# Performance work log

Measured on AMD Instinct MI355X. Metric: run time of the kernel, lower is better.

Reference implementation:

```python
import jax, jax.numpy as jnp
import numpy as np

B, NW = 1024, 300
N = NW // 3          # 100 tokens (keypoints)
E = 5                # token dim after cat of PE(2): 3 + 2
H, D, L = 4, 64, 3   # heads, d_attention, layers


def setup_inputs() -> dict:
    key = jax.random.key(0)
    ks = jax.random.split(key, 8)
    s = jnp.float32(0.1)
    x = jax.random.normal(ks[0], (B, NW), dtype=jnp.float32)
    Wq = jax.random.normal(ks[1], (L, H, D, E), dtype=jnp.float32) * s  # per-head W_Q (no bias)
    Wk = jax.random.normal(ks[2], (L, H, D, E), dtype=jnp.float32) * s
    Wv = jax.random.normal(ks[3], (L, H, D, E), dtype=jnp.float32) * s
    Wo = jax.random.normal(ks[4], (L, E, H * D), dtype=jnp.float32) * s  # MHA output proj (no bias)
    Wf = jax.random.normal(ks[5], (L, E, E), dtype=jnp.float32) * s      # FFN linear
    bf = jax.random.normal(ks[6], (L, E), dtype=jnp.float32) * s
    g1 = jnp.ones((L, E), dtype=jnp.float32)
    b1 = jnp.zeros((L, E), dtype=jnp.float32)
    g2 = jnp.ones((L, E), dtype=jnp.float32)
    b2 = jnp.zeros((L, E), dtype=jnp.float32)
    return dict(x=x, Wq=Wq, Wk=Wk, Wv=Wv, Wo=Wo, Wf=Wf, bf=bf,
                g1=g1, b1=b1, g2=g2, b2=b2)


def _layer_norm(x, g, b, eps=1e-5):
    mu = jnp.mean(x, axis=-1, keepdims=True)
    var = jnp.mean((x - mu) ** 2, axis=-1, keepdims=True)  # biased, like torch LN
    return (x - mu) / jnp.sqrt(var + eps) * g + b


def reference(x, Wq, Wk, Wv, Wo, Wf, bf, g1, b1, g2, b2):
    kp = x.reshape(B, N, 3)                      # 'b (n d) -> b n d', d=3
    mask = kp[:, :, -1] > 0                      # [B,N] keypoint confidence mask
    # PositionalEncoding(d_model=2, kind='cat'): div_term=[1] -> pe=[sin(pos),cos(pos)]
    pos = jnp.arange(N, dtype=jnp.float32)
    pe = jnp.stack([jnp.sin(pos), jnp.cos(pos)], axis=-1)         # [N,2]
    out = jnp.concatenate([kp, jnp.broadcast_to(pe, (B, N, 2))], axis=-1)  # [B,N,5]
    out = jnp.where(mask[:, :, None], out, jnp.float32(0.0))      # out[~mask]=0

    pair = mask[:, None, None, :] & mask[:, None, :, None]        # [B,1,N,N]
    neg = -jnp.finfo(jnp.float32).max
    scale = jnp.float32(1.0 / np.sqrt(D))
    for l in range(L):
        # per-head projections (heads vectorized over h)
        q = jnp.einsum('bne,hde->bhnd', out, Wq[l])
        k = jnp.einsum('bne,hde->bhnd', out, Wk[l])
        v = jnp.einsum('bne,hde->bhnd', out, Wv[l])
        dots = jnp.einsum('bhid,bhjd->bhij', q, k) * scale        # [B,H,N,N]
        dots = jnp.where(pair, dots, neg)
        attn = jax.nn.softmax(dots, axis=-1)
        o = jnp.einsum('bhij,bhjd->bhid', attn, v)                # [B,H,N,D]
        o = o.transpose(0, 2, 1, 3).reshape(B, N, H * D)          # concat heads
        attn_out = o @ Wo[l].T                                    # [B,N,E]
        ln1 = _layer_norm(attn_out + out, g1[l], b1[l])
        ffn = jax.nn.relu(ln1 @ Wf[l].T + bf[l])
        out = _layer_norm(ffn + ln1, g2[l], b2[l])
    return out
```

## Files before the change

kernel.cpp:

```cpp
#include <hip/hip_runtime.h>
#include <math.h>

#define NTOK 100
#define EDIM 5
#define NH   4
#define NL   3
#define DD   64
#define BLK  256

__device__ __forceinline__ float fexp2(float x){ float r; asm("v_exp_f32 %0, %1" : "=v"(r) : "v"(x)); return r; }
__device__ __forceinline__ float frcp (float x){ float r; asm("v_rcp_f32 %0, %1" : "=v"(r) : "v"(x)); return r; }
__device__ __forceinline__ float frsq (float x){ float r; asm("v_rsq_f32 %0, %1" : "=v"(r) : "v"(x)); return r; }
#define RL(v, l) __int_as_float(__builtin_amdgcn_readlane(__float_as_int(v), (l)))

__global__ void precompute_mp(const float* __restrict__ Wq,
                              const float* __restrict__ Wk,
                              const float* __restrict__ Wv,
                              const float* __restrict__ Wo,
                              float* __restrict__ mp) {
  const int blk = blockIdx.x;
  const int which = blk / 12;
  const int rem = blk % 12;
  const int l = rem / 4, h = rem % 4;
  const int t = threadIdx.x;

  __shared__ float A[320];
  __shared__ float Bsh[320];

  const float* wa = (which ? Wv : Wq) + (l*NH + h)*DD*EDIM;
  for (int r = t; r < 320; r += 64) A[r] = wa[r];
  if (which == 0) {
    const float* wk = Wk + (l*NH + h)*DD*EDIM;
    for (int r = t; r < 320; r += 64) Bsh[r] = wk[r];
  } else {
    for (int r = t; r < 320; r += 64) {
      int f = r >> 6, d = r & 63;
      Bsh[r] = Wo[(l*EDIM + f)*(NH*DD) + h*DD + d];
    }
  }
  __syncthreads();
  if (t < 25) {
    int e = t / 5, f = t % 5;
    float acc = 0.f;
    if (which == 0) {
      #pragma unroll 8
      for (int d = 0; d < DD; ++d) acc += A[d*5+e] * Bsh[d*5+f];
      acc *= 0.125f * 1.44269504088896340736f;
    } else {
      #pragma unroll 8
      for (int d = 0; d < DD; ++d) acc += A[d*5+e] * Bsh[f*64+d];
    }
    mp[which*960 + ((l*NH + h)*EDIM + e)*8 + f] = acc;
  }
}

__global__ __launch_bounds__(BLK, 4) void encoder_kernel(
    const float* __restrict__ x,
    const float* __restrict__ mp,
    const float* __restrict__ Wf,
    const float* __restrict__ bfv,
    const float* __restrict__ g1,
    const float* __restrict__ b1,
    const float* __restrict__ g2,
    const float* __restrict__ b2,
    float* __restrict__ out)
{
  const int b = blockIdx.x, t = threadIdx.x;
  const int wv = t >> 6, ln = t & 63;

  __shared__ float4 s_MP4[480];
  __shared__ float4 s_wp4[2][NH][104];
  __shared__ float  s_wp1[2][NH][104];
  __shared__ float4 s_i4[104];
  __shared__ float  s_i1[104];
  __shared__ int    s_cidx[NTOK];
  __shared__ unsigned long long s_bal[2];

  const float* mpf = (const float*)s_MP4;
  for (int r = t; r < 480; r += BLK) s_MP4[r] = ((const float4*)mp)[r];
  for (int r = t; r < 104; r += BLK) { s_i4[r] = make_float4(0.f,0.f,0.f,0.f); s_i1[r] = 0.f; }

  float k0=0.f, k1=0.f, k2=0.f, msk=0.f;
  if (t < NTOK) {
    k0 = x[b*300 + 3*t];
    k1 = x[b*300 + 3*t + 1];
    k2 = x[b*300 + 3*t + 2];
    msk = (k2 > 0.f) ? 1.f : 0.f;
  }
  unsigned long long bal = __ballot(t < NTOK && msk != 0.f);
  if (t == 0)  s_bal[0] = bal;
  if (t == 64) s_bal[1] = bal;
  __syncthreads();
  const unsigned long long bw0 = s_bal[0], bw1 = s_bal[1];
  const int nm = __builtin_amdgcn_readfirstlane(__popcll(bw0) + __popcll(bw1));
  if (t < NTOK) {
    int lane = t & 63;
    unsigned long long lm = (lane == 0) ? 0ull : ((1ull << lane) - 1ull);
    int pre = (t < 64) ? __popcll(bw0 & lm) : (__popcll(bw0) + __popcll(bw1 & lm));
    if (msk != 0.f) {
      s_i4[pre] = make_float4(k0, k1, k2, __sinf((float)t));
      s_i1[pre] = __cosf((float)t);
      s_cidx[t] = pre;
    } else {
      s_cidx[t] = nm;
    }
  }
  __syncthreads();

  const int rows = nm + 1;
  const bool twoRows = (rows > 64);
  const int jhiA = (nm < 64) ? nm : 64;
  const float wext = (float)(NTOK - nm);

  float oA0,oA1,oA2,oA3,oA4, oB0,oB1,oB2,oB3,oB4;
  { float4 v = s_i4[ln]; oA0=v.x; oA1=v.y; oA2=v.z; oA3=v.w; oA4=s_i1[ln]; }
  if (twoRows && ln < 40) {
    float4 v = s_i4[ln+64]; oB0=v.x; oB1=v.y; oB2=v.z; oB3=v.w; oB4=s_i1[ln+64];
  } else { oB0=0.f; oB1=0.f; oB2=0.f; oB3=0.f; oB4=0.f; }

  int bufp = 0;

  for (int l = 0; l < NL; ++l) {
    const float* Mh = mpf + ((l*NH + wv)*EDIM)*8;
    const float* Ph = mpf + 960 + ((l*NH + wv)*EDIM)*8;

    auto attn_row = [&](float o0,float o1,float o2,float o3,float o4,int row) {
      float oc[5] = {o0,o1,o2,o3,o4};
      float a0=0.f,a1=0.f,a2=0.f,a3=0.f,a4=0.f;
      #pragma unroll
      for (int e = 0; e < 5; ++e) {
        float4 mr = *(const float4*)(Mh + e*8); float m4 = Mh[e*8+4];
        a0 += oc[e]*mr.x; a1 += oc[e]*mr.y; a2 += oc[e]*mr.z;
        a3 += oc[e]*mr.w; a4 += oc[e]*m4;
      }
      const bool rep = (row == nm);
      if (rep) { a0=0.f; a1=0.f; a2=0.f; a3=0.f; a4=0.f; }
      float ls=0.f, w0=0.f, w1=0.f, w2=0.f, w3=0.f, w4=0.f;
      #pragma unroll 4
      for (int j = 0; j < jhiA; ++j) {
        float ox = RL(oA0,j), oy = RL(oA1,j), oz = RL(oA2,j),
              ow = RL(oA3,j), oe = RL(oA4,j);
        float s = (a0*ox + a1*oy) + ((a2*oz + a3*ow) + a4*oe);
        float p = fexp2(s);
        ls += p;
        w0 += p*ox; w1 += p*oy; w2 += p*oz; w3 += p*ow; w4 += p*oe;
      }
      if (twoRows) {
        #pragma unroll 4
        for (int j = 64; j < nm; ++j) {
          int jl = j - 64;
          float ox = RL(oB0,jl), oy = RL(oB1,jl), oz = RL(oB2,jl),
                ow = RL(oB3,jl), oe = RL(oB4,jl);
          float s = (a0*ox + a1*oy) + ((a2*oz + a3*ow) + a4*oe);
          float p = fexp2(s);
          ls += p;
          w0 += p*ox; w1 += p*oy; w2 += p*oz; w3 += p*ow; w4 += p*oe;
        }
      }
      if (rep) {
        w0 += wext*o0; w1 += wext*o1; w2 += wext*o2; w3 += wext*o3; w4 += wext*o4;
      }
      float inv = rep ? 0.01f : frcp(ls);
      float wc[5] = {w0*inv, w1*inv, w2*inv, w3*inv, w4*inv};
      float c0=0.f,c1=0.f,c2=0.f,c3=0.f,c4=0.f;
      #pragma unroll
      for (int e = 0; e < 5; ++e) {
        float4 pr = *(const float4*)(Ph + e*8); float p4 = Ph[e*8+4];
        c0 += wc[e]*pr.x; c1 += wc[e]*pr.y; c2 += wc[e]*pr.z;
        c3 += wc[e]*pr.w; c4 += wc[e]*p4;
      }
      if (row < rows) {
        s_wp4[bufp][wv][row] = make_float4(c0,c1,c2,c3);
        s_wp1[bufp][wv][row] = c4;
      }
    };

    attn_row(oA0,oA1,oA2,oA3,oA4, ln);
    if (twoRows) attn_row(oB0,oB1,oB2,oB3,oB4, ln+64);
    __syncthreads();

    auto upd = [&](float& p0,float& p1,float& p2,float& p3,float& p4,int row) {
      if (row >= rows) return;
      float y0=p0, y1=p1, y2=p2, y3=p3, y4=p4;
      #pragma unroll
      for (int hh = 0; hh < NH; ++hh) {
        float4 wA = s_wp4[bufp][hh][row];
        y0 += wA.x; y1 += wA.y; y2 += wA.z; y3 += wA.w;
        y4 += s_wp1[bufp][hh][row];
      }
      float yv[5] = {y0,y1,y2,y3,y4};
      float mu = 0.2f*(y0+y1+y2+y3+y4);
      float var = 0.f;
      #pragma unroll
      for (int e = 0; e < 5; ++e) { float d = yv[e]-mu; var += d*d; }
      float iv = frsq(var*0.2f + 1e-5f);
      float l1[5];
      #pragma unroll
      for (int e = 0; e < 5; ++e) l1[e] = (yv[e]-mu)*iv*g1[l*5+e] + b1[l*5+e];
      float r2[5];
      #pragma unroll
      for (int e = 0; e < 5; ++e) {
        float acc = bfv[l*5+e];
        #pragma unroll
        for (int f = 0; f < 5; ++f) acc += l1[f]*Wf[(l*5+e)*5+f];
        acc = acc > 0.f ? acc : 0.f;
        r2[e] = acc + l1[e];
      }
      float mu2 = 0.2f*(r2[0]+r2[1]+r2[2]+r2[3]+r2[4]);
      float var2 = 0.f;
      #pragma unroll
      for (int e = 0; e < 5; ++e) { float d = r2[e]-mu2; var2 += d*d; }
      float iv2 = frsq(var2*0.2f + 1e-5f);
      p0 = (r2[0]-mu2)*iv2*g2[l*5+0] + b2[l*5+0];
      p1 = (r2[1]-mu2)*iv2*g2[l*5+1] + b2[l*5+1];
      p2 = (r2[2]-mu2)*iv2*g2[l*5+2] + b2[l*5+2];
      p3 = (r2[3]-mu2)*iv2*g2[l*5+3] + b2[l*5+3];
      p4 = (r2[4]-mu2)*iv2*g2[l*5+4] + b2[l*5+4];
    };
    upd(oA0,oA1,oA2,oA3,oA4, ln);
    if (twoRows) upd(oB0,oB1,oB2,oB3,oB4, ln+64);
    bufp ^= 1;
  }

  if (wv == 0) {
    if (ln < rows) { s_i4[ln] = make_float4(oA0,oA1,oA2,oA3); s_i1[ln] = oA4; }
    if (twoRows && (ln + 64 < rows)) {
      s_i4[ln+64] = make_float4(oB0,oB1,oB2,oB3); s_i1[ln+64] = oB4;
    }
  }
  __syncthreads();
  for (int r = t; r < NTOK*EDIM; r += BLK) {
    int i = r / EDIM;
    int e = r - i*EDIM;
    int c = s_cidx[i];
    float v = (e < 4) ? ((const float*)&s_i4[c])[e] : s_i1[c];
    out[b*(NTOK*EDIM) + r] = v;
  }
}

extern "C" void kernel_launch(void* const* d_in, const int* in_sizes, int n_in,
                              void* d_out, int out_size, void* d_ws, size_t ws_size,
                              hipStream_t stream) {
  const float* x  = (const float*)d_in[0];
  const float* Wq = (const float*)d_in[1];
  const float* Wk = (const float*)d_in[2];
  const float* Wv = (const float*)d_in[3];
  const float* Wo = (const float*)d_in[4];
  const float* Wf = (const float*)d_in[5];
  const float* bf = (const float*)d_in[6];
  const float* g1 = (const float*)d_in[7];
  const float* b1 = (const float*)d_in[8];
  const float* g2 = (const float*)d_in[9];
  const float* b2 = (const float*)d_in[10];
  float* outp = (float*)d_out;
  float* mp   = (float*)d_ws;

  precompute_mp<<<24, 64, 0, stream>>>(Wq, Wk, Wv, Wo, mp);
  encoder_kernel<<<1024, BLK, 0, stream>>>(x, mp, Wf, bf, g1, b1, g2, b2, outp);
}
```

Measured before the change: 128.8 us.

## Process two heads per wave with 128-thread blocks and cache LN/FFN params in LDS

Halves the block to two waves, each computing two attention heads per row and sharing the readlane broadcasts and key loads across both heads. The cross-wave reduction now reads only the partner wave's partial sum from LDS and keeps its own in registers. Small FFN and LayerNorm parameters are staged into shared memory instead of being read from global memory per row. The doubled per-lane work raises register pressure and gives fewer waves per block to hide latency, and the second-row work is limited to lanes below 40.

```diff
diff --git a/kernel.cpp b/kernel.cpp
--- a/kernel.cpp
+++ b/kernel.cpp
@@ -6,7 +6,7 @@
 #define NH   4
 #define NL   3
 #define DD   64
-#define BLK  256
+#define BLK  128
 
 __device__ __forceinline__ float fexp2(float x){ float r; asm("v_exp_f32 %0, %1" : "=v"(r) : "v"(x)); return r; }
 __device__ __forceinline__ float frcp (float x){ float r; asm("v_rcp_f32 %0, %1" : "=v"(r) : "v"(x)); return r; }
@@ -54,7 +54,7 @@
   }
 }
 
-__global__ __launch_bounds__(BLK, 4) void encoder_kernel(
+__global__ __launch_bounds__(BLK, 2) void encoder_kernel(
     const float* __restrict__ x,
     const float* __restrict__ mp,
     const float* __restrict__ Wf,
@@ -69,16 +69,27 @@
   const int wv = t >> 6, ln = t & 63;
 
   __shared__ float4 s_MP4[480];
-  __shared__ float4 s_wp4[2][NH][104];
-  __shared__ float  s_wp1[2][NH][104];
+  __shared__ float4 s_wp4[2][2][104];
+  __shared__ float  s_wp1[2][2][104];
   __shared__ float4 s_i4[104];
   __shared__ float  s_i1[104];
+  __shared__ float  s_cf[152];
   __shared__ int    s_cidx[NTOK];
   __shared__ unsigned long long s_bal[2];
 
   const float* mpf = (const float*)s_MP4;
   for (int r = t; r < 480; r += BLK) s_MP4[r] = ((const float4*)mp)[r];
   for (int r = t; r < 104; r += BLK) { s_i4[r] = make_float4(0.f,0.f,0.f,0.f); s_i1[r] = 0.f; }
+  for (int r = t; r < 150; r += BLK) {
+    float v;
+    if      (r <  75) v = Wf[r];
+    else if (r <  90) v = bfv[r-75];
+    else if (r < 105) v = g1[r-90];
+    else if (r < 120) v = b1[r-105];
+    else if (r < 135) v = g2[r-120];
+    else              v = b2[r-135];
+    s_cf[r] = v;
+  }
 
   float k0=0.f, k1=0.f, k2=0.f, msk=0.f;
   if (t < NTOK) {
@@ -119,31 +130,45 @@
   } else { oB0=0.f; oB1=0.f; oB2=0.f; oB3=0.f; oB4=0.f; }
 
   int bufp = 0;
+  float cSA[5], cSB[5];
 
   for (int l = 0; l < NL; ++l) {
-    const float* Mh = mpf + ((l*NH + wv)*EDIM)*8;
-    const float* Ph = mpf + 960 + ((l*NH + wv)*EDIM)*8;
-
-    auto attn_row = [&](float o0,float o1,float o2,float o3,float o4,int row) {
+    const float* M0 = mpf + ((l*NH + 2*wv    )*EDIM)*8;
+    const float* M1 = mpf + ((l*NH + 2*wv + 1)*EDIM)*8;
+    const float* P0 = mpf + 960 + ((l*NH + 2*wv    )*EDIM)*8;
+    const float* P1 = mpf + 960 + ((l*NH + 2*wv + 1)*EDIM)*8;
+
+    auto attn_row = [&](float o0,float o1,float o2,float o3,float o4,
+                        int row, float (&cS)[5]) {
       float oc[5] = {o0,o1,o2,o3,o4};
-      float a0=0.f,a1=0.f,a2=0.f,a3=0.f,a4=0.f;
-      #pragma unroll
-      for (int e = 0; e < 5; ++e) {
-        float4 mr = *(const float4*)(Mh + e*8); float m4 = Mh[e*8+4];
-        a0 += oc[e]*mr.x; a1 += oc[e]*mr.y; a2 += oc[e]*mr.z;
-        a3 += oc[e]*mr.w; a4 += oc[e]*m4;
+      float a00=0.f,a01=0.f,a02=0.f,a03=0.f,a04=0.f;
+      float a10=0.f,a11=0.f,a12=0.f,a13=0.f,a14=0.f;
+      #pragma unroll
+      for (int e = 0; e < 5; ++e) {
+        float4 m0 = *(const float4*)(M0 + e*8); float m04 = M0[e*8+4];
+        float4 m1 = *(const float4*)(M1 + e*8); float m14 = M1[e*8+4];
+        float v = oc[e];
+        a00 += v*m0.x; a01 += v*m0.y; a02 += v*m0.z; a03 += v*m0.w; a04 += v*m04;
+        a10 += v*m1.x; a11 += v*m1.y; a12 += v*m1.z; a13 += v*m1.w; a14 += v*m14;
       }
       const bool rep = (row == nm);
-      if (rep) { a0=0.f; a1=0.f; a2=0.f; a3=0.f; a4=0.f; }
-      float ls=0.f, w0=0.f, w1=0.f, w2=0.f, w3=0.f, w4=0.f;
+      if (rep) {
+        a00=0.f;a01=0.f;a02=0.f;a03=0.f;a04=0.f;
+        a10=0.f;a11=0.f;a12=0.f;a13=0.f;a14=0.f;
+      }
+      float ls0=0.f, ls1=0.f;
+      float w00=0.f,w01=0.f,w02=0.f,w03=0.f,w04=0.f;
+      float w10=0.f,w11=0.f,w12=0.f,w13=0.f,w14=0.f;
       #pragma unroll 4
       for (int j = 0; j < jhiA; ++j) {
         float ox = RL(oA0,j), oy = RL(oA1,j), oz = RL(oA2,j),
               ow = RL(oA3,j), oe = RL(oA4,j);
-        float s = (a0*ox + a1*oy) + ((a2*oz + a3*ow) + a4*oe);
-        float p = fexp2(s);
-        ls += p;
-        w0 += p*ox; w1 += p*oy; w2 += p*oz; w3 += p*ow; w4 += p*oe;
+        float s0 = (a00*ox + a01*oy) + ((a02*oz + a03*ow) + a04*oe);
+        float s1 = (a10*ox + a11*oy) + ((a12*oz + a13*ow) + a14*oe);
+        float p0 = fexp2(s0), p1 = fexp2(s1);
+        ls0 += p0; ls1 += p1;
+        w00 += p0*ox; w01 += p0*oy; w02 += p0*oz; w03 += p0*ow; w04 += p0*oe;
+        w10 += p1*ox; w11 += p1*oy; w12 += p1*oz; w13 += p1*ow; w14 += p1*oe;
       }
       if (twoRows) {
         #pragma unroll 4
@@ -151,43 +176,52 @@
           int jl = j - 64;
           float ox = RL(oB0,jl), oy = RL(oB1,jl), oz = RL(oB2,jl),
                 ow = RL(oB3,jl), oe = RL(oB4,jl);
-          float s = (a0*ox + a1*oy) + ((a2*oz + a3*ow) + a4*oe);
-          float p = fexp2(s);
-          ls += p;
-          w0 += p*ox; w1 += p*oy; w2 += p*oz; w3 += p*ow; w4 += p*oe;
+          float s0 = (a00*ox + a01*oy) + ((a02*oz + a03*ow) + a04*oe);
+          float s1 = (a10*ox + a11*oy) + ((a12*oz + a13*ow) + a14*oe);
+          float p0 = fexp2(s0), p1 = fexp2(s1);
+          ls0 += p0; ls1 += p1;
+          w00 += p0*ox; w01 += p0*oy; w02 += p0*oz; w03 += p0*ow; w04 += p0*oe;
+          w10 += p1*ox; w11 += p1*oy; w12 += p1*oz; w13 += p1*ow; w14 += p1*oe;
         }
       }
       if (rep) {
-        w0 += wext*o0; w1 += wext*o1; w2 += wext*o2; w3 += wext*o3; w4 += wext*o4;
-      }
-      float inv = rep ? 0.01f : frcp(ls);
-      float wc[5] = {w0*inv, w1*inv, w2*inv, w3*inv, w4*inv};
+        w00 += wext*o0; w01 += wext*o1; w02 += wext*o2; w03 += wext*o3; w04 += wext*o4;
+        w10 += wext*o0; w11 += wext*o1; w12 += wext*o2; w13 += wext*o3; w14 += wext*o4;
+      }
+      float inv0 = rep ? 0.01f : frcp(ls0);
+      float inv1 = rep ? 0.01f : frcp(ls1);
+      float wc0[5] = {w00*inv0, w01*inv0, w02*inv0, w03*inv0, w04*inv0};
+      float wc1[5] = {w10*inv1, w11*inv1, w12*inv1, w13*inv1, w14*inv1};
       float c0=0.f,c1=0.f,c2=0.f,c3=0.f,c4=0.f;
       #pragma unroll
       for (int e = 0; e < 5; ++e) {
-        float4 pr = *(const float4*)(Ph + e*8); float p4 = Ph[e*8+4];
-        c0 += wc[e]*pr.x; c1 += wc[e]*pr.y; c2 += wc[e]*pr.z;
-        c3 += wc[e]*pr.w; c4 += wc[e]*p4;
-      }
-      if (row < rows) {
-        s_wp4[bufp][wv][row] = make_float4(c0,c1,c2,c3);
-        s_wp1[bufp][wv][row] = c4;
-      }
+        float4 pr = *(const float4*)(P0 + e*8); float p4 = P0[e*8+4];
+        c0 += wc0[e]*pr.x; c1 += wc0[e]*pr.y; c2 += wc0[e]*pr.z;
+        c3 += wc0[e]*pr.w; c4 += wc0[e]*p4;
+      }
+      #pragma unroll
+      for (int e = 0; e < 5; ++e) {
+        float4 pr = *(const float4*)(P1 + e*8); float p4 = P1[e*8+4];
+        c0 += wc1[e]*pr.x; c1 += wc1[e]*pr.y; c2 += wc1[e]*pr.z;
+        c3 += wc1[e]*pr.w; c4 += wc1[e]*p4;
+      }
+      cS[0]=c0; cS[1]=c1; cS[2]=c2; cS[3]=c3; cS[4]=c4;
+      s_wp4[bufp][wv][row] = make_float4(c0,c1,c2,c3);
+      s_wp1[bufp][wv][row] = c4;
     };
 
-    attn_row(oA0,oA1,oA2,oA3,oA4, ln);
-    if (twoRows) attn_row(oB0,oB1,oB2,oB3,oB4, ln+64);
+    attn_row(oA0,oA1,oA2,oA3,oA4, ln, cSA);
+    if (twoRows && ln < 40) attn_row(oB0,oB1,oB2,oB3,oB4, ln+64, cSB);
     __syncthreads();
 
-    auto upd = [&](float& p0,float& p1,float& p2,float& p3,float& p4,int row) {
+    auto upd = [&](float& p0,float& p1,float& p2,float& p3,float& p4,
+                   float (&cS)[5], int row) {
       if (row >= rows) return;
-      float y0=p0, y1=p1, y2=p2, y3=p3, y4=p4;
-      #pragma unroll
-      for (int hh = 0; hh < NH; ++hh) {
-        float4 wA = s_wp4[bufp][hh][row];
-        y0 += wA.x; y1 += wA.y; y2 += wA.z; y3 += wA.w;
-        y4 += s_wp1[bufp][hh][row];
-      }
+      float4 wo = s_wp4[bufp][wv^1][row];
+      float wo4 = s_wp1[bufp][wv^1][row];
+      float y0 = p0 + cS[0] + wo.x,  y1 = p1 + cS[1] + wo.y;
+      float y2 = p2 + cS[2] + wo.z,  y3 = p3 + cS[3] + wo.w;
+      float y4 = p4 + cS[4] + wo4;
       float yv[5] = {y0,y1,y2,y3,y4};
       float mu = 0.2f*(y0+y1+y2+y3+y4);
       float var = 0.f;
@@ -196,13 +230,14 @@
       float iv = frsq(var*0.2f + 1e-5f);
       float l1[5];
       #pragma unroll
-      for (int e = 0; e < 5; ++e) l1[e] = (yv[e]-mu)*iv*g1[l*5+e] + b1[l*5+e];
+      for (int e = 0; e < 5; ++e)
+        l1[e] = (yv[e]-mu)*iv*s_cf[90+l*5+e] + s_cf[105+l*5+e];
       float r2[5];
       #pragma unroll
       for (int e = 0; e < 5; ++e) {
-        float acc = bfv[l*5+e];
+        float acc = s_cf[75+l*5+e];
         #pragma unroll
-        for (int f = 0; f < 5; ++f) acc += l1[f]*Wf[(l*5+e)*5+f];
+        for (int f = 0; f < 5; ++f) acc += l1[f]*s_cf[l*25+e*5+f];
         acc = acc > 0.f ? acc : 0.f;
         r2[e] = acc + l1[e];
       }
@@ -211,14 +246,14 @@
       #pragma unroll
       for (int e = 0; e < 5; ++e) { float d = r2[e]-mu2; var2 += d*d; }
       float iv2 = frsq(var2*0.2f + 1e-5f);
-      p0 = (r2[0]-mu2)*iv2*g2[l*5+0] + b2[l*5+0];
-      p1 = (r2[1]-mu2)*iv2*g2[l*5+1] + b2[l*5+1];
-      p2 = (r2[2]-mu2)*iv2*g2[l*5+2] + b2[l*5+2];
-      p3 = (r2[3]-mu2)*iv2*g2[l*5+3] + b2[l*5+3];
-      p4 = (r2[4]-mu2)*iv2*g2[l*5+4] + b2[l*5+4];
+      p0 = (r2[0]-mu2)*iv2*s_cf[120+l*5+0] + s_cf[135+l*5+0];
+      p1 = (r2[1]-mu2)*iv2*s_cf[120+l*5+1] + s_cf[135+l*5+1];
+      p2 = (r2[2]-mu2)*iv2*s_cf[120+l*5+2] + s_cf[135+l*5+2];
+      p3 = (r2[3]-mu2)*iv2*s_cf[120+l*5+3] + s_cf[135+l*5+3];
+      p4 = (r2[4]-mu2)*iv2*s_cf[120+l*5+4] + s_cf[135+l*5+4];
     };
-    upd(oA0,oA1,oA2,oA3,oA4, ln);
-    if (twoRows) upd(oB0,oB1,oB2,oB3,oB4, ln+64);
+    upd(oA0,oA1,oA2,oA3,oA4, cSA, ln);
+    if (twoRows && ln < 40) upd(oB0,oB1,oB2,oB3,oB4, cSB, ln+64);
     bufp ^= 1;
   }
 
```

After: 131.0 us. No clear change (+1.7%).
